# Optimization experiments

Hardware: AMD Instinct MI355X
Metric: run time of the kernel (lower is better)

The kernel has to match this reference:

```python
import jax, jax.numpy as jnp
import numpy as np

N_USERS, N_ITEMS, N_GENRES = 31360, 6807, 18
TOTAL = N_USERS + N_ITEMS + N_GENRES          # 38185
OFFSET = TOTAL - N_GENRES                      # 38167
D = 16                                         # embedding_dim
B = 524288                                     # batch
MLP_DIMS = [64, 32, 16]
IN_DIM = 3 * D                                 # field_num * embedding_dim


def setup_inputs() -> dict:
    key = jax.random.key(0)
    ks = jax.random.split(key, 14)
    user = jax.random.randint(ks[0], (B, 1), 0, N_USERS)
    item = N_USERS + jax.random.randint(ks[1], (B, 1), 0, N_ITEMS)
    x_onehot = jnp.concatenate([user, item], axis=1)            # [B,2] global ids
    multi_hot = jax.random.randint(ks[2], (B, N_GENRES), 0, 2)  # [B,18] 0/1 mask
    s = 0.05
    emb_table = s * jax.random.normal(ks[3], (TOTAL, D), jnp.float32)
    fc_table = s * jax.random.normal(ks[4], (TOTAL, 1), jnp.float32)
    W1 = s * jax.random.normal(ks[5], (IN_DIM, MLP_DIMS[0]), jnp.float32)
    b1 = jnp.zeros((MLP_DIMS[0],), jnp.float32)
    W2 = s * jax.random.normal(ks[6], (MLP_DIMS[0], MLP_DIMS[1]), jnp.float32)
    b2 = jnp.zeros((MLP_DIMS[1],), jnp.float32)
    W3 = s * jax.random.normal(ks[7], (MLP_DIMS[1], MLP_DIMS[2]), jnp.float32)
    b3 = jnp.zeros((MLP_DIMS[2],), jnp.float32)
    W4 = s * jax.random.normal(ks[8], (MLP_DIMS[2], 1), jnp.float32)
    b4 = jnp.zeros((1,), jnp.float32)
    bias = jnp.zeros((1,), jnp.float32)
    return {"x_onehot": x_onehot, "multi_hot": multi_hot,
            "emb_table": emb_table, "fc_table": fc_table,
            "W1": W1, "b1": b1, "W2": W2, "b2": b2,
            "W3": W3, "b3": b3, "W4": W4, "b4": b4, "bias": bias}


def reference(x_onehot, multi_hot, emb_table, fc_table,
              W1, b1, W2, b2, W3, b3, W4, b4, bias):
    mh = multi_hot.astype(emb_table.dtype)                      # [B,18]
    # ragged multi-hot sum == mask @ genre slice of table (EmbeddingBag sum)
    embed_mh = mh @ emb_table[OFFSET:]                          # [B,D]
    embed_x = jnp.concatenate(
        [emb_table[x_onehot], embed_mh[:, None, :]], axis=1)    # [B,3,D]
    fc_mh = mh @ fc_table[OFFSET:]                              # [B,1]
    fc_x = jnp.concatenate(
        [fc_table[x_onehot], fc_mh[:, None, :]], axis=1)        # [B,3,1]
    # FM second-order term
    sum_e = embed_x.sum(axis=1)                                 # [B,D]
    fm_y = bias + fc_x.sum(axis=1) + 0.5 * jnp.sum(
        sum_e ** 2 - (embed_x ** 2).sum(axis=1), axis=1, keepdims=True)  # [B,1]
    # MLP (dropout inactive at inference)
    h = embed_x.reshape(embed_x.shape[0], -1)                   # [B,48]
    h = jax.nn.relu(h @ W1 + b1)
    h = jax.nn.relu(h @ W2 + b2)
    h = jax.nn.relu(h @ W3 + b3)
    mlp_y = h @ W4 + b4                                         # [B,1]
    return jax.nn.sigmoid(fm_y[:, 0] + mlp_y[:, 0])             # [B]
```

## Files before the change

### kernel.cpp

```cpp
#include <hip/hip_runtime.h>
#include <hip/hip_bf16.h>

namespace {

constexpr int kBatch  = 524288;
constexpr int kD      = 16;
constexpr int kOffset = 38167;
constexpr int kNG     = 18;

constexpr int W1B0   = 0;
constexpr int W2B0   = 8192;
constexpr int W3B0   = 12288;
constexpr int GB0    = 13312;
constexpr int WBYTES = 14336;

typedef __attribute__((ext_vector_type(8))) short short8;
typedef __attribute__((ext_vector_type(4))) float f32x4;

__device__ __forceinline__ unsigned short f2bf(float f) {
    return __builtin_bit_cast(unsigned short, __float2bfloat16(f));
}
__device__ __forceinline__ unsigned pk2(float a, float b) {
    return (unsigned)f2bf(a) | ((unsigned)f2bf(b) << 16);
}
__device__ __forceinline__ float bf2f(unsigned short s) {
    union { unsigned u; float f; } v; v.u = ((unsigned)s) << 16;
    return v.f;
}

__global__ void prep_weights(const float* __restrict__ emb,
                             const float* __restrict__ W1,
                             const float* __restrict__ W2,
                             const float* __restrict__ W3,
                             unsigned short* __restrict__ wimg)
{
    const int t = (int)threadIdx.x;
    for (int i = t; i < WBYTES / 2; i += 256) wimg[i] = 0;
    __syncthreads();
    for (int i = t; i < 48 * 64; i += 256) {
        int k = i >> 6, n = i & 63;
        int byte = W1B0 + n * 128 + ((k * 2) ^ ((n & 7) << 4));
        wimg[byte >> 1] = f2bf(W1[k * 64 + n]);
    }
    for (int i = t; i < 64 * 32; i += 256) {
        int k = i >> 5, n = i & 31;
        int byte = W2B0 + n * 128 + ((k * 2) ^ ((n & 7) << 4));
        wimg[byte >> 1] = f2bf(W2[k * 32 + n]);
    }
    for (int i = t; i < 32 * 16; i += 256) {
        int k = i >> 4, n = i & 15;
        int byte = W3B0 + n * 64 + ((k * 2) ^ ((n & 3) << 4));
        wimg[byte >> 1] = f2bf(W3[k * 16 + n]);
    }
    for (int i = t; i < 512; i += 256) {
        int c = i >> 5, r = i & 31, g = r >> 3, j = r & 7;
        int kg = 8 * g + j;
        wimg[(GB0 >> 1) + (4 * c + g) * 8 + j] =
            (kg < kNG) ? f2bf(emb[(size_t)(kOffset + kg) * kD + c]) : (unsigned short)0;
    }
}

__global__ __launch_bounds__(256, 3) void deepfm_fwd(
    const int*   __restrict__ x_onehot,
    const int*   __restrict__ multi_hot,
    const float* __restrict__ emb,
    const float* __restrict__ fc,
    const unsigned short* __restrict__ wimg,
    const float* __restrict__ b1,
    const float* __restrict__ b2,
    const float* __restrict__ b3,
    const float* __restrict__ W4,
    const float* __restrict__ b4,
    const float* __restrict__ bias,
    float*       __restrict__ out)
{
    __shared__ alignas(16) unsigned short s_w[WBYTES / 2];
    __shared__ alignas(16) unsigned short s_act[4 * 4096];

    const int t = (int)threadIdx.x;

    {
        const uint4* src = reinterpret_cast<const uint4*>(wimg);
        uint4*       dst = reinterpret_cast<uint4*>(s_w);
        #pragma unroll
        for (int q = 0; q < 4; ++q) {
            const int idx = t + 256 * q;
            if (idx < WBYTES / 16) dst[idx] = src[idx];
        }
    }

    const int i    = (int)blockIdx.x * 256 + t;
    const int lane = t & 63;
    const int w    = t >> 6;
    const int c    = lane & 15, g = lane >> 4;
    char* __restrict__ awc = (char*)(s_act + w * 4096);
    const char* __restrict__ swc = (const char*)s_w;

    const int l7 = lane & 7;
    const int sb = lane * 128;
    int rA[2];
    #pragma unroll
    for (int kt = 0; kt < 2; ++kt)
        rA[kt] = c * 128 + (((4 * kt + g) ^ (c & 7)) << 4);
    int wad[4][4];
    #pragma unroll
    for (int r = 0; r < 4; ++r) {
        const int Xlo  = (r & 1) << 4;
        const int Xhi  = (2 * (g & 1) + (r >> 1)) << 5;
        const int rowb = (4 * g + r) * 128 + ((2 * c) ^ Xlo);
        #pragma unroll
        for (int nt = 0; nt < 4; ++nt)
            wad[r][nt] = rowb + ((32 * nt) ^ Xhi);
    }
    const int rW3 = W3B0 + c * 64 + ((g ^ (c & 3)) << 4);

    int2 mh[9];
    {
        const int2* mh2 = reinterpret_cast<const int2*>(multi_hot + (size_t)kNG * i);
        #pragma unroll
        for (int q = 0; q < 9; ++q) mh[q] = mh2[q];
    }
    const int2 ids = *reinterpret_cast<const int2*>(x_onehot + 2 * (size_t)i);

    float h[32];
    {
        const float4* eu = reinterpret_cast<const float4*>(emb + (size_t)ids.x * kD);
        #pragma unroll
        for (int q = 0; q < 4; ++q) {
            const float4 a = eu[q];
            h[4*q+0] = a.x; h[4*q+1] = a.y; h[4*q+2] = a.z; h[4*q+3] = a.w;
        }
        const float4* ei = reinterpret_cast<const float4*>(emb + (size_t)ids.y * kD);
        #pragma unroll
        for (int q = 0; q < 4; ++q) {
            const float4 a = ei[q];
            h[16+4*q+0] = a.x; h[16+4*q+1] = a.y; h[16+4*q+2] = a.z; h[16+4*q+3] = a.w;
        }
    }

    float b1v[4];
    #pragma unroll
    for (int nt = 0; nt < 4; ++nt) b1v[nt] = b1[16 * nt + c];
    float b2v[2]; b2v[0] = b2[c]; b2v[1] = b2[16 + c];
    const float b3v = b3[c];

    float lin = bias[0] + b4[0] + fc[ids.x] + fc[ids.y];
    #pragma unroll
    for (int q = 0; q < 9; ++q) {
        lin += mh[q].x ? fc[kOffset + 2 * q]     : 0.f;
        lin += mh[q].y ? fc[kOffset + 2 * q + 1] : 0.f;
    }

    {
        unsigned mw[9];
        #pragma unroll
        for (int q = 0; q < 9; ++q)
            mw[q] = (mh[q].x ? 0x3F80u : 0u) | (mh[q].y ? 0x3F800000u : 0u);
        uint4 v0; v0.x = mw[0]; v0.y = mw[1]; v0.z = mw[2]; v0.w = mw[3];
        uint4 v1; v1.x = mw[4]; v1.y = mw[5]; v1.z = mw[6]; v1.w = mw[7];
        uint4 v2; v2.x = mw[8]; v2.y = 0u;    v2.z = 0u;    v2.w = 0u;
        uint4 vz; vz.x = vz.y = vz.z = vz.w = 0u;
        *reinterpret_cast<uint4*>(awc + sb + (((0 ^ l7)) << 4)) = v0;
        *reinterpret_cast<uint4*>(awc + sb + (((1 ^ l7)) << 4)) = v1;
        *reinterpret_cast<uint4*>(awc + sb + (((2 ^ l7)) << 4)) = v2;
        *reinterpret_cast<uint4*>(awc + sb + (((3 ^ l7)) << 4)) = vz;
        *reinterpret_cast<uint4*>(awc + sb + (((6 ^ l7)) << 4)) = vz;
        *reinterpret_cast<uint4*>(awc + sb + (((7 ^ l7)) << 4)) = vz;
    }

    __syncthreads();

    const f32x4 z4 = {0.f, 0.f, 0.f, 0.f};

    {
        const short8 bfrag = *reinterpret_cast<const short8*>(s_w + (GB0 >> 1) + (4 * c + g) * 8);
        short8 af[4];
        #pragma unroll
        for (int mt = 0; mt < 4; ++mt)
            af[mt] = *reinterpret_cast<const short8*>(awc + rA[0] + 2048 * mt);
        f32x4 accb[4];
        #pragma unroll
        for (int mt = 0; mt < 4; ++mt)
            accb[mt] = __builtin_amdgcn_mfma_f32_16x16x32_bf16(af[mt], bfrag, z4, 0, 0, 0);
        #pragma unroll
        for (int mt = 0; mt < 4; ++mt)
            #pragma unroll
            for (int r = 0; r < 4; ++r)
                *reinterpret_cast<unsigned short*>(awc + wad[r][2] + 2048 * mt) = f2bf(accb[mt][r]);
    }

    {
        #pragma unroll
        for (int q = 0; q < 4; ++q) {
            uint4 d;
            d.x = pk2(h[8*q+0], h[8*q+1]);
            d.y = pk2(h[8*q+2], h[8*q+3]);
            d.z = pk2(h[8*q+4], h[8*q+5]);
            d.w = pk2(h[8*q+6], h[8*q+7]);
            *reinterpret_cast<uint4*>(awc + sb + ((q ^ l7) << 4)) = d;
        }
    }

    float fm = 0.f;
    {
        const uint4 p0 = *reinterpret_cast<const uint4*>(awc + sb + ((4 ^ l7) << 4));
        const uint4 p1 = *reinterpret_cast<const uint4*>(awc + sb + ((5 ^ l7) << 4));
        const unsigned pp[8] = {p0.x, p0.y, p0.z, p0.w, p1.x, p1.y, p1.z, p1.w};
        float em[16];
        #pragma unroll
        for (int j = 0; j < 8; ++j) {
            em[2*j+0] = bf2f((unsigned short)(pp[j] & 0xFFFFu));
            em[2*j+1] = bf2f((unsigned short)(pp[j] >> 16));
        }
        #pragma unroll
        for (int d = 0; d < kD; ++d) fm = fmaf(h[d], h[16 + d], fm);
        #pragma unroll
        for (int d = 0; d < kD; ++d) fm = fmaf(h[d] + h[16 + d], em[d], fm);
    }

    f32x4 acc1[4][4];
    #pragma unroll
    for (int mt = 0; mt < 4; ++mt)
        #pragma unroll
        for (int nt = 0; nt < 4; ++nt) acc1[mt][nt] = z4;
    #pragma unroll
    for (int kt = 0; kt < 2; ++kt) {
        short8 af[4], bfr[4];
        #pragma unroll
        for (int mt = 0; mt < 4; ++mt)
            af[mt] = *reinterpret_cast<const short8*>(awc + rA[kt] + 2048 * mt);
        #pragma unroll
        for (int nt = 0; nt < 4; ++nt)
            bfr[nt] = *reinterpret_cast<const short8*>(swc + W1B0 + rA[kt] + 2048 * nt);
        #pragma unroll
        for (int mt = 0; mt < 4; ++mt)
            #pragma unroll
            for (int nt = 0; nt < 4; ++nt)
                acc1[mt][nt] = __builtin_amdgcn_mfma_f32_16x16x32_bf16(af[mt], bfr[nt], acc1[mt][nt], 0, 0, 0);
    }
    #pragma unroll
    for (int mt = 0; mt < 4; ++mt)
        #pragma unroll
        for (int nt = 0; nt < 4; ++nt)
            #pragma unroll
            for (int r = 0; r < 4; ++r) {
                const float v = fmaxf(acc1[mt][nt][r] + b1v[nt], 0.f);
                *reinterpret_cast<unsigned short*>(awc + wad[r][nt] + 2048 * mt) = f2bf(v);
            }

    f32x4 acc2[4][2];
    #pragma unroll
    for (int mt = 0; mt < 4; ++mt)
        #pragma unroll
        for (int nt = 0; nt < 2; ++nt) acc2[mt][nt] = z4;
    #pragma unroll
    for (int kt = 0; kt < 2; ++kt) {
        short8 af[4], bfr[2];
        #pragma unroll
        for (int mt = 0; mt < 4; ++mt)
            af[mt] = *reinterpret_cast<const short8*>(awc + rA[kt] + 2048 * mt);
        #pragma unroll
        for (int nt = 0; nt < 2; ++nt)
            bfr[nt] = *reinterpret_cast<const short8*>(swc + W2B0 + rA[kt] + 2048 * nt);
        #pragma unroll
        for (int mt = 0; mt < 4; ++mt)
            #pragma unroll
            for (int nt = 0; nt < 2; ++nt)
                acc2[mt][nt] = __builtin_amdgcn_mfma_f32_16x16x32_bf16(af[mt], bfr[nt], acc2[mt][nt], 0, 0, 0);
    }
    #pragma unroll
    for (int mt = 0; mt < 4; ++mt)
        #pragma unroll
        for (int nt = 0; nt < 2; ++nt)
            #pragma unroll
            for (int r = 0; r < 4; ++r) {
                const float v = fmaxf(acc2[mt][nt][r] + b2v[nt], 0.f);
                *reinterpret_cast<unsigned short*>(awc + wad[r][nt] + 2048 * mt) = f2bf(v);
            }

    f32x4 acc3[4];
    #pragma unroll
    for (int mt = 0; mt < 4; ++mt) acc3[mt] = z4;
    {
        const short8 bfr = *reinterpret_cast<const short8*>(swc + rW3);
        short8 af[4];
        #pragma unroll
        for (int mt = 0; mt < 4; ++mt)
            af[mt] = *reinterpret_cast<const short8*>(awc + rA[0] + 2048 * mt);
        #pragma unroll
        for (int mt = 0; mt < 4; ++mt)
            acc3[mt] = __builtin_amdgcn_mfma_f32_16x16x32_bf16(af[mt], bfr, acc3[mt], 0, 0, 0);
    }
    #pragma unroll
    for (int mt = 0; mt < 4; ++mt)
        #pragma unroll
        for (int r = 0; r < 4; ++r) {
            const float v = fmaxf(acc3[mt][r] + b3v, 0.f);
            *reinterpret_cast<unsigned short*>(awc + wad[r][0] + 2048 * mt) = f2bf(v);
        }

    float mlp = 0.f;
    {
        const uint4 p0 = *reinterpret_cast<const uint4*>(awc + sb + ((0 ^ l7) << 4));
        const uint4 p1 = *reinterpret_cast<const uint4*>(awc + sb + ((1 ^ l7) << 4));
        const unsigned pp[8] = {p0.x, p0.y, p0.z, p0.w, p1.x, p1.y, p1.z, p1.w};
        #pragma unroll
        for (int j = 0; j < 8; ++j) {
            mlp = fmaf(bf2f((unsigned short)(pp[j] & 0xFFFFu)), W4[2*j],     mlp);
            mlp = fmaf(bf2f((unsigned short)(pp[j] >> 16)),     W4[2*j + 1], mlp);
        }
    }

    const float x = lin + fm + mlp;
    out[i] = 1.0f / (1.0f + __expf(-x));
}

}

extern "C" void kernel_launch(void* const* d_in, const int* in_sizes, int n_in,
                              void* d_out, int out_size, void* d_ws, size_t ws_size,
                              hipStream_t stream) {
    (void)in_sizes; (void)n_in; (void)ws_size; (void)out_size;
    const int*   x_onehot  = (const int*)  d_in[0];
    const int*   multi_hot = (const int*)  d_in[1];
    const float* emb       = (const float*)d_in[2];
    const float* fc        = (const float*)d_in[3];
    const float* W1        = (const float*)d_in[4];
    const float* b1        = (const float*)d_in[5];
    const float* W2        = (const float*)d_in[6];
    const float* b2        = (const float*)d_in[7];
    const float* W3        = (const float*)d_in[8];
    const float* b3        = (const float*)d_in[9];
    const float* W4        = (const float*)d_in[10];
    const float* b4        = (const float*)d_in[11];
    const float* biasp     = (const float*)d_in[12];
    float* out = (float*)d_out;
    unsigned short* wimg = (unsigned short*)d_ws;

    hipLaunchKernelGGL(prep_weights, dim3(1), dim3(256), 0, stream,
                       emb, W1, W2, W3, wimg);
    hipLaunchKernelGGL(deepfm_fwd, dim3(kBatch / 256), dim3(256), 0, stream,
                       x_onehot, multi_hot, emb, fc, wimg,
                       b1, b2, b3, W4, b4, biasp, out);
}
```

Measured before the change: 39.73 us.

## Swap MFMA operand roles so epilogue writes packed 8-byte LDS stores

New measurement: 42.44 us. +6.8%, slower.

```diff
diff --git a/kernel.cpp b/kernel.cpp
--- a/kernel.cpp
+++ b/kernel.cpp
@@ -102,17 +102,10 @@
     #pragma unroll
     for (int kt = 0; kt < 2; ++kt)
         rA[kt] = c * 128 + (((4 * kt + g) ^ (c & 7)) << 4);
-    int wad[4][4];
-    #pragma unroll
-    for (int r = 0; r < 4; ++r) {
-        const int Xlo  = (r & 1) << 4;
-        const int Xhi  = (2 * (g & 1) + (r >> 1)) << 5;
-        const int rowb = (4 * g + r) * 128 + ((2 * c) ^ Xlo);
-        #pragma unroll
-        for (int nt = 0; nt < 4; ++nt)
-            wad[r][nt] = rowb + ((32 * nt) ^ Xhi);
-    }
-    const int rW3 = W3B0 + c * 64 + ((g ^ (c & 3)) << 4);
+    int wepi[4];
+    #pragma unroll
+    for (int nt = 0; nt < 4; ++nt)
+        wepi[nt] = c * 128 + ((((2 * nt + (g >> 1)) ^ (c & 7))) << 4) + 8 * (g & 1);
 
     int2 mh[9];
     {
@@ -138,11 +131,15 @@
         }
     }
 
-    float b1v[4];
-    #pragma unroll
-    for (int nt = 0; nt < 4; ++nt) b1v[nt] = b1[16 * nt + c];
-    float b2v[2]; b2v[0] = b2[c]; b2v[1] = b2[16 + c];
-    const float b3v = b3[c];
+    float4 b1q[4];
+    #pragma unroll
+    for (int nt = 0; nt < 4; ++nt)
+        b1q[nt] = *reinterpret_cast<const float4*>(b1 + 16 * nt + 4 * g);
+    float4 b2q[2];
+    #pragma unroll
+    for (int nt = 0; nt < 2; ++nt)
+        b2q[nt] = *reinterpret_cast<const float4*>(b2 + 16 * nt + 4 * g);
+    const float4 b3q = *reinterpret_cast<const float4*>(b3 + 4 * g);
 
     float lin = bias[0] + b4[0] + fc[ids.x] + fc[ids.y];
     #pragma unroll
@@ -173,20 +170,19 @@
     const f32x4 z4 = {0.f, 0.f, 0.f, 0.f};
 
     {
-        const short8 bfrag = *reinterpret_cast<const short8*>(s_w + (GB0 >> 1) + (4 * c + g) * 8);
-        short8 af[4];
-        #pragma unroll
-        for (int mt = 0; mt < 4; ++mt)
-            af[mt] = *reinterpret_cast<const short8*>(awc + rA[0] + 2048 * mt);
-        f32x4 accb[4];
-        #pragma unroll
-        for (int mt = 0; mt < 4; ++mt)
-            accb[mt] = __builtin_amdgcn_mfma_f32_16x16x32_bf16(af[mt], bfrag, z4, 0, 0, 0);
-        #pragma unroll
-        for (int mt = 0; mt < 4; ++mt)
-            #pragma unroll
-            for (int r = 0; r < 4; ++r)
-                *reinterpret_cast<unsigned short*>(awc + wad[r][2] + 2048 * mt) = f2bf(accb[mt][r]);
+        const short8 gfrag = *reinterpret_cast<const short8*>(s_w + (GB0 >> 1) + (4 * c + g) * 8);
+        short8 bm[4];
+        #pragma unroll
+        for (int st = 0; st < 4; ++st)
+            bm[st] = *reinterpret_cast<const short8*>(awc + rA[0] + 2048 * st);
+        #pragma unroll
+        for (int st = 0; st < 4; ++st) {
+            const f32x4 accb = __builtin_amdgcn_mfma_f32_16x16x32_bf16(gfrag, bm[st], z4, 0, 0, 0);
+            uint2 dv;
+            dv.x = pk2(accb[0], accb[1]);
+            dv.y = pk2(accb[2], accb[3]);
+            *reinterpret_cast<uint2*>(awc + wepi[2] + 2048 * st) = dv;
+        }
     }
 
     {
@@ -220,84 +216,86 @@
 
     f32x4 acc1[4][4];
     #pragma unroll
-    for (int mt = 0; mt < 4; ++mt)
-        #pragma unroll
-        for (int nt = 0; nt < 4; ++nt) acc1[mt][nt] = z4;
+    for (int nt = 0; nt < 4; ++nt)
+        #pragma unroll
+        for (int st = 0; st < 4; ++st) acc1[nt][st] = z4;
     #pragma unroll
     for (int kt = 0; kt < 2; ++kt) {
-        short8 af[4], bfr[4];
-        #pragma unroll
-        for (int mt = 0; mt < 4; ++mt)
-            af[mt] = *reinterpret_cast<const short8*>(awc + rA[kt] + 2048 * mt);
+        short8 aW[4], bA[4];
         #pragma unroll
         for (int nt = 0; nt < 4; ++nt)
-            bfr[nt] = *reinterpret_cast<const short8*>(swc + W1B0 + rA[kt] + 2048 * nt);
-        #pragma unroll
-        for (int mt = 0; mt < 4; ++mt)
-            #pragma unroll
-            for (int nt = 0; nt < 4; ++nt)
-                acc1[mt][nt] = __builtin_amdgcn_mfma_f32_16x16x32_bf16(af[mt], bfr[nt], acc1[mt][nt], 0, 0, 0);
-    }
-    #pragma unroll
-    for (int mt = 0; mt < 4; ++mt)
+            aW[nt] = *reinterpret_cast<const short8*>(swc + W1B0 + rA[kt] + 2048 * nt);
+        #pragma unroll
+        for (int st = 0; st < 4; ++st)
+            bA[st] = *reinterpret_cast<const short8*>(awc + rA[kt] + 2048 * st);
         #pragma unroll
         for (int nt = 0; nt < 4; ++nt)
             #pragma unroll
-            for (int r = 0; r < 4; ++r) {
-                const float v = fmaxf(acc1[mt][nt][r] + b1v[nt], 0.f);
-                *reinterpret_cast<unsigned short*>(awc + wad[r][nt] + 2048 * mt) = f2bf(v);
-            }
-
-    f32x4 acc2[4][2];
-    #pragma unroll
-    for (int mt = 0; mt < 4; ++mt)
-        #pragma unroll
-        for (int nt = 0; nt < 2; ++nt) acc2[mt][nt] = z4;
+            for (int st = 0; st < 4; ++st)
+                acc1[nt][st] = __builtin_amdgcn_mfma_f32_16x16x32_bf16(aW[nt], bA[st], acc1[nt][st], 0, 0, 0);
+    }
+    #pragma unroll
+    for (int nt = 0; nt < 4; ++nt)
+        #pragma unroll
+        for (int st = 0; st < 4; ++st) {
+            const float v0 = fmaxf(acc1[nt][st][0] + b1q[nt].x, 0.f);
+            const float v1 = fmaxf(acc1[nt][st][1] + b1q[nt].y, 0.f);
+            const float v2 = fmaxf(acc1[nt][st][2] + b1q[nt].z, 0.f);
+            const float v3 = fmaxf(acc1[nt][st][3] + b1q[nt].w, 0.f);
+            uint2 dv; dv.x = pk2(v0, v1); dv.y = pk2(v2, v3);
+            *reinterpret_cast<uint2*>(awc + wepi[nt] + 2048 * st) = dv;
+        }
+
+    f32x4 acc2[2][4];
+    #pragma unroll
+    for (int nt = 0; nt < 2; ++nt)
+        #pragma unroll
+        for (int st = 0; st < 4; ++st) acc2[nt][st] = z4;
     #pragma unroll
     for (int kt = 0; kt < 2; ++kt) {
-        short8 af[4], bfr[2];
-        #pragma unroll
-        for (int mt = 0; mt < 4; ++mt)
-            af[mt] = *reinterpret_cast<const short8*>(awc + rA[kt] + 2048 * mt);
+        short8 aW[2], bA[4];
         #pragma unroll
         for (int nt = 0; nt < 2; ++nt)
-            bfr[nt] = *reinterpret_cast<const short8*>(swc + W2B0 + rA[kt] + 2048 * nt);
-        #pragma unroll
-        for (int mt = 0; mt < 4; ++mt)
-            #pragma unroll
-            for (int nt = 0; nt < 2; ++nt)
-                acc2[mt][nt] = __builtin_amdgcn_mfma_f32_16x16x32_bf16(af[mt], bfr[nt], acc2[mt][nt], 0, 0, 0);
-    }
-    #pragma unroll
-    for (int mt = 0; mt < 4; ++mt)
+            aW[nt] = *reinterpret_cast<const short8*>(swc + W2B0 + rA[kt] + 2048 * nt);
+        #pragma unroll
+        for (int st = 0; st < 4; ++st)
+            bA[st] = *reinterpret_cast<const short8*>(awc + rA[kt] + 2048 * st);
         #pragma unroll
         for (int nt = 0; nt < 2; ++nt)
             #pragma unroll
-            for (int r = 0; r < 4; ++r) {
-                const float v = fmaxf(acc2[mt][nt][r] + b2v[nt], 0.f);
-                *reinterpret_cast<unsigned short*>(awc + wad[r][nt] + 2048 * mt) = f2bf(v);
-            }
-
-    f32x4 acc3[4];
-    #pragma unroll
-    for (int mt = 0; mt < 4; ++mt) acc3[mt] = z4;
-    {
-        const short8 bfr = *reinterpret_cast<const short8*>(swc + rW3);
-        short8 af[4];
-        #pragma unroll
-        for (int mt = 0; mt < 4; ++mt)
-            af[mt] = *reinterpret_cast<const short8*>(awc + rA[0] + 2048 * mt);
-        #pragma unroll
-        for (int mt = 0; mt < 4; ++mt)
-            acc3[mt] = __builtin_amdgcn_mfma_f32_16x16x32_bf16(af[mt], bfr, acc3[mt], 0, 0, 0);
-    }
-    #pragma unroll
-    for (int mt = 0; mt < 4; ++mt)
-        #pragma unroll
-        for (int r = 0; r < 4; ++r) {
-            const float v = fmaxf(acc3[mt][r] + b3v, 0.f);
-            *reinterpret_cast<unsigned short*>(awc + wad[r][0] + 2048 * mt) = f2bf(v);
-        }
+            for (int st = 0; st < 4; ++st)
+                acc2[nt][st] = __builtin_amdgcn_mfma_f32_16x16x32_bf16(aW[nt], bA[st], acc2[nt][st], 0, 0, 0);
+    }
+    #pragma unroll
+    for (int nt = 0; nt < 2; ++nt)
+        #pragma unroll
+        for (int st = 0; st < 4; ++st) {
+            const float v0 = fmaxf(acc2[nt][st][0] + b2q[nt].x, 0.f);
+            const float v1 = fmaxf(acc2[nt][st][1] + b2q[nt].y, 0.f);
+            const float v2 = fmaxf(acc2[nt][st][2] + b2q[nt].z, 0.f);
+            const float v3 = fmaxf(acc2[nt][st][3] + b2q[nt].w, 0.f);
+            uint2 dv; dv.x = pk2(v0, v1); dv.y = pk2(v2, v3);
+            *reinterpret_cast<uint2*>(awc + wepi[nt] + 2048 * st) = dv;
+        }
+
+    {
+        const short8 aW = *reinterpret_cast<const short8*>(
+            swc + W3B0 + c * 64 + ((g ^ (c & 3)) << 4));
+        short8 bA[4];
+        #pragma unroll
+        for (int st = 0; st < 4; ++st)
+            bA[st] = *reinterpret_cast<const short8*>(awc + rA[0] + 2048 * st);
+        #pragma unroll
+        for (int st = 0; st < 4; ++st) {
+            const f32x4 a3 = __builtin_amdgcn_mfma_f32_16x16x32_bf16(aW, bA[st], z4, 0, 0, 0);
+            const float v0 = fmaxf(a3[0] + b3q.x, 0.f);
+            const float v1 = fmaxf(a3[1] + b3q.y, 0.f);
+            const float v2 = fmaxf(a3[2] + b3q.z, 0.f);
+            const float v3 = fmaxf(a3[3] + b3q.w, 0.f);
+            uint2 dv; dv.x = pk2(v0, v1); dv.y = pk2(v2, v3);
+            *reinterpret_cast<uint2*>(awc + wepi[0] + 2048 * st) = dv;
+        }
+    }
 
     float mlp = 0.f;
     {
```
